# Kernel optimization log

Measured on AMD Instinct MI355X. Metric: run time of the kernel, lower is better.

The kernel has to match this reference:

```python
import jax, jax.numpy as jnp
import numpy as np

N = 8192        # nodes
D = 256         # embedding_dim
H = 64          # nhid
DEG = 32        # neighbors per node
E = N * DEG     # edges
NTYPES = 16
NEG = -9e15


def setup_inputs() -> dict:
    key = jax.random.key(0)
    ks = jax.random.split(key, 8)
    x = jax.random.normal(ks[0], (N, D), jnp.float32)
    # linear params (torch nn.Linear convention: W [out,in])
    sc = 1.0 / np.sqrt(D)
    Wq = jax.random.uniform(ks[1], (H, D), jnp.float32, -sc, sc)
    bq = jax.random.uniform(ks[2], (H,), jnp.float32, -sc, sc)
    Wk = jax.random.uniform(ks[3], (H, D), jnp.float32, -sc, sc)
    bk = jax.random.uniform(ks[4], (H,), jnp.float32, -sc, sc)
    Wv = jax.random.uniform(ks[5], (H, D), jnp.float32, -sc, sc)
    edge_k_table = jax.random.normal(ks[6], (NTYPES, 1), jnp.float32)
    # deterministic graph: each node i has DEG distinct neighbors, sorted per row
    # so that row-major nonzero order of adj matches the edge list order.
    dst = np.sort((np.arange(N)[:, None] + 13 * np.arange(1, DEG + 1)[None, :]) % N, axis=1)
    src = np.repeat(np.arange(N), DEG)
    dst = dst.reshape(-1)
    adj = np.zeros((N, N), np.float32)
    adj[src, dst] = 1.0
    edge_index = jnp.asarray(np.stack([src, dst]), jnp.int32)  # [2, E]
    edge_type = jax.random.randint(ks[7], (E,), 0, NTYPES, jnp.int32)
    return {"x": x, "adj": jnp.asarray(adj), "edge_index": edge_index,
            "edge_type": edge_type, "Wq": Wq, "bq": bq, "Wk": Wk, "bk": bk,
            "Wv": Wv, "edge_k_table": edge_k_table}


def reference(x, adj, edge_index, edge_type, Wq, bq, Wk, bk, Wv, edge_k_table):
    Q = x @ Wq.T + bq                       # [N, H]
    K = x @ Wk.T + bk                       # [N, H]
    V = x @ Wv.T                            # [N, H]
    S = Q @ K.T                             # [N, N] dense scores
    ek = edge_k_table[edge_type].reshape(-1)  # [E] scalar edge biases
    S = S.at[edge_index[0], edge_index[1]].add(ek)
    S = S / H
    S = jnp.where(adj > 0, S, NEG)
    S = S / np.float32(np.sqrt(H))
    P = jax.nn.softmax(S, axis=1)
    return P @ V                            # [N, H]
```

## Files before the change

kernel.cpp:

```cpp
#include <hip/hip_runtime.h>

#define N_NODES 8192
#define DIM     256
#define NH      64
#define DEG     32
#define G       4

__global__ __launch_bounds__(64) void qkv_kernel(
    const float* __restrict__ x,
    const float* __restrict__ Wq, const float* __restrict__ bq,
    const float* __restrict__ Wk, const float* __restrict__ bk,
    const float* __restrict__ Wv,
    float* __restrict__ Q, float* __restrict__ K, float* __restrict__ V)
{
    const int g0 = blockIdx.x * G;
    const int t  = threadIdx.x;

    __shared__ float xs[G * DIM];

    const float4* xin = (const float4*)(x + (size_t)g0 * DIM);
    float4* xs4 = (float4*)xs;
    #pragma unroll
    for (int c = 0; c < (G * DIM / 4) / 64; ++c)
        xs4[t + 64 * c] = xin[t + 64 * c];
    __syncthreads();

    const float4* wq = (const float4*)(Wq + t * DIM);
    const float4* wk = (const float4*)(Wk + t * DIM);
    const float4* wv = (const float4*)(Wv + t * DIM);

    float accq[G], acck[G], accv[G];
    #pragma unroll
    for (int m = 0; m < G; ++m) { accq[m] = 0.f; acck[m] = 0.f; accv[m] = 0.f; }

    #pragma unroll 4
    for (int c = 0; c < DIM / 4; ++c) {
        const float4 aq = wq[c];
        const float4 ak = wk[c];
        const float4 av = wv[c];
        #pragma unroll
        for (int m = 0; m < G; ++m) {
            const float4 xv = ((const float4*)(xs + m * DIM))[c];
            accq[m] += xv.x * aq.x + xv.y * aq.y + xv.z * aq.z + xv.w * aq.w;
            acck[m] += xv.x * ak.x + xv.y * ak.y + xv.z * ak.z + xv.w * ak.w;
            accv[m] += xv.x * av.x + xv.y * av.y + xv.z * av.z + xv.w * av.w;
        }
    }

    const float bqv = bq[t];
    const float bkv = bk[t];
    #pragma unroll
    for (int m = 0; m < G; ++m) {
        const int o = (g0 + m) * NH + t;
        Q[o] = accq[m] + bqv;
        K[o] = acck[m] + bkv;
        V[o] = accv[m];
    }
}

__global__ __launch_bounds__(64) void attn_kernel(
    const float* __restrict__ Q, const float* __restrict__ K,
    const float* __restrict__ V,
    const int* __restrict__ edge_dst,
    const int* __restrict__ edge_type,
    const float* __restrict__ ektab,
    float* __restrict__ out)
{
    const int i = blockIdx.x;
    const int t = threadIdx.x;

    __shared__ float qs[NH];
    qs[t] = Q[i * NH + t];
    __syncthreads();

    float s = -1e30f;
    int nbr = 0;
    if (t < DEG) {
        const int e = i * DEG + t;
        nbr = edge_dst[e];
        const float ek = ektab[edge_type[e]];
        const float4* kr = (const float4*)(K + (size_t)nbr * NH);
        const float4* q4 = (const float4*)qs;
        float acc = 0.f;
        #pragma unroll
        for (int d = 0; d < NH / 4; ++d) {
            const float4 kv = kr[d];
            const float4 qv = q4[d];
            acc += qv.x * kv.x + qv.y * kv.y + qv.z * kv.z + qv.w * kv.w;
        }
        s = (acc + ek) * (1.0f / 512.0f);
    }

    float m = s;
    #pragma unroll
    for (int off = 32; off > 0; off >>= 1) m = fmaxf(m, __shfl_xor(m, off));
    float p = __expf(s - m);
    float l = p;
    #pragma unroll
    for (int off = 32; off > 0; off >>= 1) l += __shfl_xor(l, off);
    p /= l;

    float o = 0.f;
    #pragma unroll 8
    for (int j = 0; j < DEG; ++j) {
        const float pj = __shfl(p, j);
        const int   nj = __shfl(nbr, j);
        o += pj * V[(size_t)nj * NH + t];
    }

    out[i * NH + t] = o;
}

extern "C" void kernel_launch(void* const* d_in, const int* in_sizes, int n_in,
                              void* d_out, int out_size, void* d_ws, size_t ws_size,
                              hipStream_t stream) {
    const float* x     = (const float*)d_in[0];
    const int*   eidx  = (const int*)d_in[2];
    const int*   etyp  = (const int*)d_in[3];
    const float* Wq    = (const float*)d_in[4];
    const float* bq    = (const float*)d_in[5];
    const float* Wk    = (const float*)d_in[6];
    const float* bk    = (const float*)d_in[7];
    const float* Wv    = (const float*)d_in[8];
    const float* ektab = (const float*)d_in[9];
    float*       out   = (float*)d_out;

    const int E = in_sizes[2] / 2;

    float* Q = (float*)d_ws;
    float* K = Q + (size_t)N_NODES * NH;
    float* V = K + (size_t)N_NODES * NH;

    qkv_kernel<<<dim3(N_NODES / G), dim3(64), 0, stream>>>(x, Wq, bq, Wk, bk, Wv, Q, K, V);
    attn_kernel<<<dim3(N_NODES), dim3(64), 0, stream>>>(Q, K, V, eidx + E, etyp, ektab, out);
}
```

Baseline: 377.5 us.

## Split QKV projection reduction across two waves with LDS combine and larger row group

The QKV projection kernel now processes 8 rows per block instead of 4, so each weight load is reused across more rows. It uses 128 threads, two waves that each cover half of the 256-wide input dimension. Partial sums are exchanged through shared memory and each wave writes half of the rows. This is meant to cut global weight traffic per row and expose more parallelism per block, at the cost of an extra barrier, LDS traffic, and half as many blocks.

Result: faster. 357.7 us (-5.2%).

```diff
diff --git a/kernel.cpp b/kernel.cpp
--- a/kernel.cpp
+++ b/kernel.cpp
@@ -4,9 +4,9 @@
 #define DIM     256
 #define NH      64
 #define DEG     32
-#define G       4
+#define G       8
 
-__global__ __launch_bounds__(64) void qkv_kernel(
+__global__ __launch_bounds__(128) void qkv_kernel(
     const float* __restrict__ x,
     const float* __restrict__ Wq, const float* __restrict__ bq,
     const float* __restrict__ Wk, const float* __restrict__ bk,
@@ -14,47 +14,61 @@
     float* __restrict__ Q, float* __restrict__ K, float* __restrict__ V)
 {
     const int g0 = blockIdx.x * G;
-    const int t  = threadIdx.x;
+    const int t  = threadIdx.x & 63;
+    const int w  = threadIdx.x >> 6;
 
     __shared__ float xs[G * DIM];
+    __shared__ float red[3][G][64];
 
     const float4* xin = (const float4*)(x + (size_t)g0 * DIM);
     float4* xs4 = (float4*)xs;
     #pragma unroll
-    for (int c = 0; c < (G * DIM / 4) / 64; ++c)
-        xs4[t + 64 * c] = xin[t + 64 * c];
+    for (int c = 0; c < (G * DIM / 4) / 128; ++c)
+        xs4[threadIdx.x + 128 * c] = xin[threadIdx.x + 128 * c];
     __syncthreads();
 
-    const float4* wq = (const float4*)(Wq + t * DIM);
-    const float4* wk = (const float4*)(Wk + t * DIM);
-    const float4* wv = (const float4*)(Wv + t * DIM);
+    const int c0 = w * (DIM / 4 / 2);
+    const float4* wq = (const float4*)(Wq + t * DIM) + c0;
+    const float4* wk = (const float4*)(Wk + t * DIM) + c0;
+    const float4* wv = (const float4*)(Wv + t * DIM) + c0;
 
     float accq[G], acck[G], accv[G];
     #pragma unroll
     for (int m = 0; m < G; ++m) { accq[m] = 0.f; acck[m] = 0.f; accv[m] = 0.f; }
 
     #pragma unroll 4
-    for (int c = 0; c < DIM / 4; ++c) {
+    for (int c = 0; c < DIM / 4 / 2; ++c) {
         const float4 aq = wq[c];
         const float4 ak = wk[c];
         const float4 av = wv[c];
         #pragma unroll
         for (int m = 0; m < G; ++m) {
-            const float4 xv = ((const float4*)(xs + m * DIM))[c];
+            const float4 xv = ((const float4*)(xs + m * DIM))[c0 + c];
             accq[m] += xv.x * aq.x + xv.y * aq.y + xv.z * aq.z + xv.w * aq.w;
             acck[m] += xv.x * ak.x + xv.y * ak.y + xv.z * ak.z + xv.w * ak.w;
             accv[m] += xv.x * av.x + xv.y * av.y + xv.z * av.z + xv.w * av.w;
         }
     }
 
+    const int other0 = (1 - w) * (G / 2);
+    #pragma unroll
+    for (int m = 0; m < G / 2; ++m) {
+        red[0][other0 + m][t] = accq[other0 + m];
+        red[1][other0 + m][t] = acck[other0 + m];
+        red[2][other0 + m][t] = accv[other0 + m];
+    }
+    __syncthreads();
+
     const float bqv = bq[t];
     const float bkv = bk[t];
+    const int mine0 = w * (G / 2);
     #pragma unroll
-    for (int m = 0; m < G; ++m) {
-        const int o = (g0 + m) * NH + t;
-        Q[o] = accq[m] + bqv;
-        K[o] = acck[m] + bkv;
-        V[o] = accv[m];
+    for (int m = 0; m < G / 2; ++m) {
+        const int slot = mine0 + m;
+        const int o = (g0 + slot) * NH + t;
+        Q[o] = accq[slot] + red[0][slot][t] + bqv;
+        K[o] = acck[slot] + red[1][slot][t] + bkv;
+        V[o] = accv[slot] + red[2][slot][t];
     }
 }
 
@@ -131,6 +145,6 @@
     float* K = Q + (size_t)N_NODES * NH;
     float* V = K + (size_t)N_NODES * NH;
 
-    qkv_kernel<<<dim3(N_NODES / G), dim3(64), 0, stream>>>(x, Wq, bq, Wk, bk, Wv, Q, K, V);
+    qkv_kernel<<<dim3(N_NODES / G), dim3(128), 0, stream>>>(x, Wq, bq, Wk, bk, Wv, Q, K, V);
     attn_kernel<<<dim3(N_NODES), dim3(64), 0, stream>>>(Q, K, V, eidx + E, etyp, ektab, out);
 }
```
